# Kernel optimization log

Measured on AMD Instinct MI355X. Metric: run time of the kernel, lower is better.

## Reference

```python
import jax, jax.numpy as jnp
import numpy as np

BETA = 0.9
TH = 1.0  # snn.Leaky default threshold
SPARSITY = 0.5


@jax.custom_vjp
def spike(x):
    # Heaviside spike; surrogate (atan, alpha=2) gradient as in snntorch default
    return (x > 0).astype(x.dtype)

def _spike_fwd(x):
    return spike(x), x

def _spike_bwd(x, g):
    return (g / (1.0 + (jnp.pi * x) ** 2),)

spike.defvjp(_spike_fwd, _spike_bwd)


def setup_inputs() -> dict:
    key = jax.random.key(0)
    ks = jax.random.split(key, 6)
    T, B, NIN, NH, NOUT = 50, 512, 784, 1000, 10

    def mk_w(k, o, i):
        k1, k2 = jax.random.split(k)
        w = jax.random.normal(k1, (o, i), jnp.float32) * (1.0 / np.sqrt(i))
        mask = (jax.random.uniform(k2, (o, i)) > SPARSITY).astype(jnp.float32)
        return w * mask

    x = jax.random.normal(ks[0], (T, B, NIN), jnp.float32)
    return dict(
        x=x,
        W0=mk_w(ks[1], NH, NIN), b0=jnp.zeros((NH,), jnp.float32),
        W1=mk_w(ks[2], NH, NH), b1=jnp.zeros((NH,), jnp.float32),
        W2=mk_w(ks[3], NH, NH), b2=jnp.zeros((NH,), jnp.float32),
        W3=mk_w(ks[4], NOUT, NH), b3=jnp.zeros((NOUT,), jnp.float32),
    )


def reference(x, W0, b0, W1, b1, W2, b2, W3, b3):
    params = ((W0, b0), (W1, b1), (W2, b2), (W3, b3))
    B = x.shape[1]
    mems0 = tuple(jnp.zeros((B, W.shape[0]), x.dtype) for W, _ in params)

    def step(mems, xt):
        inp = xt
        new_mems, spks = [], []
        for (W, b), m in zip(params, mems):
            cur = inp @ W.T + b
            # snntorch Leaky (reset_mechanism='subtract'):
            # reset from previous mem (detached), then mem = beta*mem + I - reset*th
            reset = jax.lax.stop_gradient((m > TH).astype(x.dtype))
            m_new = BETA * m + cur - reset * TH
            s = spike(m_new - TH)
            new_mems.append(m_new)
            spks.append(s)
            inp = s
        return tuple(new_mems), (tuple(spks), tuple(new_mems))

    _, (spk_rec, mem_rec) = jax.lax.scan(step, mems0, x)
    # spk_rec/mem_rec: tuples of [T, B, dim] arrays per layer
    return (*spk_rec, *mem_rec)
```

## Files before the change

### kernel.cpp

```cpp
#include <hip/hip_runtime.h>


typedef int int4v  __attribute__((ext_vector_type(4)));
typedef int int16v __attribute__((ext_vector_type(16)));

#define XSCALE 68719476736.0
#define WSCALE 1099511627776.0
#define TC 10

__global__ void wsplit_i8(const float* __restrict__ W, signed char* __restrict__ out,
                          int Nreal, int Npad, int K, int Kpad)
{
    int idx = blockIdx.x * blockDim.x + threadIdx.x;
    int total = Npad * Kpad;
    if (idx >= total) return;
    int n = idx / Kpad, k = idx - n * Kpad;
    long long v = 0;
    if (n < Nreal && k < K) v = __double2ll_rn((double)W[(size_t)n * K + k] * WSCALE);
    size_t plane = (size_t)total;
#pragma unroll
    for (int p = 0; p < 4; ++p) {
        int d = (int)(v & 255); if (d > 127) d -= 256;
        out[p * plane + idx] = (signed char)d;
        v = (v - d) >> 8;
    }
    out[4 * plane + idx] = (signed char)v;
}

__global__ void xsplit_chunk(const float* __restrict__ x, signed char* __restrict__ out)
{
    int idx = blockIdx.x * blockDim.x + threadIdx.x;
    if (idx >= 5120 * 832) return;
    int row = idx / 832, k = idx - row * 832;
    long long v = 0;
    if (k < 784) v = __double2ll_rn((double)x[(size_t)row * 784 + k] * XSCALE);
    const size_t plane = (size_t)5120 * 832;
    signed char* o = out + idx;
#pragma unroll
    for (int p = 0; p < 4; ++p) {
        int d = (int)(v & 255); if (d > 127) d -= 256;
        o[p * plane] = (signed char)d;
        v = (v - d) >> 8;
    }
    o[4 * plane] = (signed char)v;
}

template<int NA, int KP, int CS>
__global__ __launch_bounds__(256)
void gemm32(const signed char* __restrict__ Ap, size_t planeA,
            const signed char* __restrict__ Wp, size_t planeW,
            double* __restrict__ curout)
{
    __shared__ __align__(16) signed char Wld[5 * 64 * 80];
    __shared__ __align__(16) signed char Ald[NA * 64 * 80];
    constexpr int NIT = KP / 64;

    const int tid = threadIdx.x;
    const int l   = tid & 63;
    const int w   = tid >> 6;
    const int wm  = (w & 1) * 32;
    const int wn  = (w >> 1) * 32;
    const int r32 = l & 31;
    const int h   = l >> 5;

    const int bm = blockIdx.y * 64;
    const int bn = blockIdx.x * 64;

    const int srow = tid >> 2;
    const int sc   = (tid & 3) * 16;

    const signed char* ag = Ap + (size_t)(bm + srow) * KP + sc;
    const signed char* wg = Wp + (size_t)(bn + srow) * KP + sc;

    int4v Ar[NA], Wr[5];
#pragma unroll
    for (int p = 0; p < 5; ++p)  Wr[p] = *(const int4v*)(wg + p * planeW);
#pragma unroll
    for (int p = 0; p < NA; ++p) Ar[p] = *(const int4v*)(ag + p * planeA);

    int16v acc[5];
#pragma unroll
    for (int s = 0; s < 5; ++s)
#pragma unroll
        for (int r = 0; r < 16; ++r) acc[s][r] = 0;

    for (int it = 0; it < NIT; ++it) {
        __syncthreads();
#pragma unroll
        for (int p = 0; p < 5; ++p)
            *(int4v*)&Wld[(p * 64 + srow) * 80 + sc] = Wr[p];
#pragma unroll
        for (int p = 0; p < NA; ++p)
            *(int4v*)&Ald[(p * 64 + srow) * 80 + sc] = Ar[p];
        __syncthreads();

        if (it + 1 < NIT) {
            int kb = (it + 1) * 64;
#pragma unroll
            for (int p = 0; p < 5; ++p)
                Wr[p] = *(const int4v*)(wg + kb + p * planeW);
#pragma unroll
            for (int p = 0; p < NA; ++p)
                Ar[p] = *(const int4v*)(ag + kb + p * planeA);
        }

#pragma unroll
        for (int k2 = 0; k2 < 2; ++k2) {
            const int off = k2 * 32 + 16 * h;
            if constexpr (NA == 5) {
                int4v af[5], bq[5];
#pragma unroll
                for (int p = 0; p < 5; ++p)
                    af[p] = *(const int4v*)&Ald[(p * 64 + wm + r32) * 80 + off];
#pragma unroll
                for (int q = 0; q < 5; ++q)
                    bq[q] = *(const int4v*)&Wld[(q * 64 + wn + r32) * 80 + off];
#pragma unroll
                for (int q = 0; q < 5; ++q)
#pragma unroll
                    for (int p = 0; p < 5; ++p)
                        if (p + q >= 4)
                            acc[p + q - 4] = __builtin_amdgcn_mfma_i32_32x32x32_i8(
                                af[p], bq[q], acc[p + q - 4], 0, 0, 0);
            } else {
                int4v a0 = *(const int4v*)&Ald[(wm + r32) * 80 + off];
#pragma unroll
                for (int q = 0; q < 5; ++q) {
                    int4v bq = *(const int4v*)&Wld[(q * 64 + wn + r32) * 80 + off];
                    acc[q] = __builtin_amdgcn_mfma_i32_32x32x32_i8(a0, bq, acc[q], 0, 0, 0);
                }
            }
        }
    }

    const int col = bn + wn + r32;
    if (col < CS) {
#pragma unroll
        for (int reg = 0; reg < 16; ++reg) {
            int row = bm + wm + (reg & 3) + 8 * (reg >> 2) + 4 * h;
            double v = (double)acc[4][reg];
            v = v * 256.0 + (double)acc[3][reg];
            v = v * 256.0 + (double)acc[2][reg];
            v = v * 256.0 + (double)acc[1][reg];
            v = v * 256.0 + (double)acc[0][reg];
            curout[(size_t)row * CS + col] = v * (NA == 5 ? 0x1p-44 : 0x1p-40);
        }
    }
}

template<int KP>
__global__ __launch_bounds__(256)
void gemm32w(const signed char* __restrict__ Asp,
             const signed char* __restrict__ Wp, size_t planeW,
             double* __restrict__ curout)
{
    __shared__ __align__(16) signed char Wld[5 * 64 * 80];
    __shared__ __align__(16) signed char Ald[128 * 80];
    constexpr int NIT = KP / 64;

    const int tid = threadIdx.x;
    const int l   = tid & 63;
    const int w   = tid >> 6;
    const int wm  = (w & 1) * 64;
    const int wn  = (w >> 1) * 32;
    const int r32 = l & 31;
    const int h   = l >> 5;

    const int bm = blockIdx.y * 128;
    const int bn = blockIdx.x * 64;

    const int srA = tid >> 1;
    const int scA = (tid & 1) * 32;
    const int srW = tid >> 2;
    const int scW = (tid & 3) * 16;

    const signed char* ag = Asp + (size_t)(bm + srA) * KP + scA;
    const signed char* wg = Wp  + (size_t)(bn + srW) * KP + scW;

    int4v Ar0 = *(const int4v*)(ag);
    int4v Ar1 = *(const int4v*)(ag + 16);
    int4v Wr[5];
#pragma unroll
    for (int p = 0; p < 5; ++p) Wr[p] = *(const int4v*)(wg + p * planeW);

    int16v acc[2][5];
#pragma unroll
    for (int mi = 0; mi < 2; ++mi)
#pragma unroll
        for (int s = 0; s < 5; ++s)
#pragma unroll
            for (int r = 0; r < 16; ++r) acc[mi][s][r] = 0;

    for (int it = 0; it < NIT; ++it) {
        __syncthreads();
#pragma unroll
        for (int p = 0; p < 5; ++p)
            *(int4v*)&Wld[(p * 64 + srW) * 80 + scW] = Wr[p];
        *(int4v*)&Ald[srA * 80 + scA]      = Ar0;
        *(int4v*)&Ald[srA * 80 + scA + 16] = Ar1;
        __syncthreads();

        if (it + 1 < NIT) {
            int kb = (it + 1) * 64;
            Ar0 = *(const int4v*)(ag + kb);
            Ar1 = *(const int4v*)(ag + kb + 16);
#pragma unroll
            for (int p = 0; p < 5; ++p)
                Wr[p] = *(const int4v*)(wg + kb + p * planeW);
        }

#pragma unroll
        for (int k2 = 0; k2 < 2; ++k2) {
            const int off = k2 * 32 + 16 * h;
            int4v bq[5];
#pragma unroll
            for (int q = 0; q < 5; ++q)
                bq[q] = *(const int4v*)&Wld[(q * 64 + wn + r32) * 80 + off];
#pragma unroll
            for (int mi = 0; mi < 2; ++mi) {
                int4v a0 = *(const int4v*)&Ald[(wm + mi * 32 + r32) * 80 + off];
#pragma unroll
                for (int q = 0; q < 5; ++q)
                    acc[mi][q] = __builtin_amdgcn_mfma_i32_32x32x32_i8(
                        a0, bq[q], acc[mi][q], 0, 0, 0);
            }
        }
    }

    const int col = bn + wn + r32;
#pragma unroll
    for (int mi = 0; mi < 2; ++mi)
#pragma unroll
        for (int reg = 0; reg < 16; ++reg) {
            int row = bm + wm + mi * 32 + (reg & 3) + 8 * (reg >> 2) + 4 * h;
            double v = (double)acc[mi][4][reg];
            v = v * 256.0 + (double)acc[mi][3][reg];
            v = v * 256.0 + (double)acc[mi][2][reg];
            v = v * 256.0 + (double)acc[mi][1][reg];
            v = v * 256.0 + (double)acc[mi][0][reg];
            curout[(size_t)row * 1024 + col] = v * 0x1p-40;
        }
}

__global__ __launch_bounds__(256)
void if_update(const double* __restrict__ cur, const float* __restrict__ bias,
               double* __restrict__ mw, float* __restrict__ spk,
               float* __restrict__ mem, signed char* __restrict__ spk_i8,
               int first)
{
    int idx = blockIdx.x * blockDim.x + threadIdx.x;
    if (idx >= 512 * 500) return;
    int row = idx / 500, col = (idx - row * 500) * 2;
    double2 mp = first ? make_double2(0.0, 0.0)
                       : *(const double2*)&mw[(size_t)row * 1000 + col];
    double bs0 = (double)bias[col], bs1 = (double)bias[col + 1];
#pragma unroll 2
    for (int t = 0; t < TC; ++t) {
        double2 c = *(const double2*)&cur[((size_t)t * 512 + row) * 1024 + col];
        double rst0 = (mp.x > 1.0) ? 1.0 : 0.0;
        double rst1 = (mp.y > 1.0) ? 1.0 : 0.0;
        double mn0 = 0.9 * mp.x + (c.x + bs0) - rst0;
        double mn1 = 0.9 * mp.y + (c.y + bs1) - rst1;
        int s0 = (mn0 > 1.0) ? 1 : 0;
        int s1 = (mn1 > 1.0) ? 1 : 0;
        size_t o = ((size_t)t * 512 + row) * 1000 + col;
        *(float2*)&spk[o] = make_float2((float)s0, (float)s1);
        *(float2*)&mem[o] = make_float2((float)mn0, (float)mn1);
        *(short*)&spk_i8[((size_t)t * 512 + row) * 1024 + col] =
            (short)(s0 | (s1 << 8));
        mp.x = mn0; mp.y = mn1;
    }
    *(double2*)&mw[(size_t)row * 1000 + col] = mp;
}

__global__ __launch_bounds__(256)
void if3_kernel(const double* __restrict__ cur3, const float* __restrict__ bias,
                float* __restrict__ spk3, float* __restrict__ mem3)
{
    int idx = blockIdx.x * blockDim.x + threadIdx.x;
    if (idx >= 5120) return;
    int brow = idx / 10, col = idx - brow * 10;
    double bs = (double)bias[col];
    double mp = 0.0;
    for (int t = 0; t < 50; ++t) {
        double c   = cur3[((size_t)t * 512 + brow) * 16 + col] + bs;
        double rst = (mp > 1.0) ? 1.0 : 0.0;
        double mn  = 0.9 * mp + c - rst;
        size_t o   = (size_t)t * 5120 + (size_t)brow * 10 + col;
        spk3[o] = (mn > 1.0) ? 1.0f : 0.0f;
        mem3[o] = (float)mn;
        mp = mn;
    }
}

extern "C" void kernel_launch(void* const* d_in, const int* in_sizes, int n_in,
                              void* d_out, int out_size, void* d_ws, size_t ws_size,
                              hipStream_t stream)
{
    const float* x  = (const float*)d_in[0];
    const float* W0 = (const float*)d_in[1];
    const float* b0 = (const float*)d_in[2];
    const float* W1 = (const float*)d_in[3];
    const float* b1 = (const float*)d_in[4];
    const float* W2 = (const float*)d_in[5];
    const float* b2 = (const float*)d_in[6];
    const float* W3 = (const float*)d_in[7];
    const float* b3 = (const float*)d_in[8];
    float* out = (float*)d_out;

    const int T = 50;
    const size_t LNH = (size_t)512 * 1000;
    const size_t LNO = (size_t)512 * 10;

    float* spk0 = out;
    float* spk1 = spk0 + (size_t)T * LNH;
    float* spk2 = spk1 + (size_t)T * LNH;
    float* spk3 = spk2 + (size_t)T * LNH;
    float* mem0 = spk3 + (size_t)T * LNO;
    float* mem1 = mem0 + (size_t)T * LNH;
    float* mem2 = mem1 + (size_t)T * LNH;
    float* mem3 = mem2 + (size_t)T * LNH;

    double* cur = (double*)d_ws;
    double* mw0 = cur + (size_t)5120 * 1024;
    double* mw1 = mw0 + LNH;
    double* mw2 = mw1 + LNH;
    signed char* W0d = (signed char*)(mw2 + LNH);
    signed char* W1d = W0d + (size_t)5 * 1024 * 832;
    signed char* W2d = W1d + (size_t)5 * 1024 * 1024;
    signed char* W3d = W2d + (size_t)5 * 1024 * 1024;
    signed char* xsb = W3d + (size_t)5 * 64 * 1024;
    signed char* sp0 = xsb + (size_t)5 * 5120 * 832;
    signed char* sp1 = sp0 + (size_t)5120 * 1024;
    signed char* sp2 = sp1 + (size_t)5120 * 1024;

    hipMemsetAsync(sp0, 0, (size_t)2 * 5120 * 1024 + (size_t)25600 * 1024, stream);

    wsplit_i8<<<(1024 * 832  + 255) / 256, 256, 0, stream>>>(W0, W0d, 1000, 1024, 784,  832);
    wsplit_i8<<<(1024 * 1024 + 255) / 256, 256, 0, stream>>>(W1, W1d, 1000, 1024, 1000, 1024);
    wsplit_i8<<<(1024 * 1024 + 255) / 256, 256, 0, stream>>>(W2, W2d, 1000, 1024, 1000, 1024);
    wsplit_i8<<<(64 * 1024   + 255) / 256, 256, 0, stream>>>(W3, W3d, 10,   64,   1000, 1024);

    const size_t plA0 = (size_t)5120 * 832;
    const size_t plW0 = (size_t)1024 * 832;
    const size_t plWH = (size_t)1024 * 1024;
    const size_t plW3 = (size_t)64 * 1024;

    dim3 blk(256);
    dim3 g0(16, 80);
    dim3 gW(16, 40);
    dim3 g3(1, 400);

    for (int c = 0; c < T / TC; ++c) {
        const int t0 = c * TC;
        const int first = (c == 0);

        xsplit_chunk<<<(5120 * 832 + 255) / 256, 256, 0, stream>>>(
            x + (size_t)t0 * 512 * 784, xsb);

        gemm32<5, 832, 1024><<<g0, blk, 0, stream>>>(xsb, plA0, W0d, plW0, cur);
        if_update<<<1000, 256, 0, stream>>>(cur, b0, mw0,
            spk0 + (size_t)t0 * LNH, mem0 + (size_t)t0 * LNH, sp0, first);

        gemm32w<1024><<<gW, blk, 0, stream>>>(sp0, W1d, plWH, cur);
        if_update<<<1000, 256, 0, stream>>>(cur, b1, mw1,
            spk1 + (size_t)t0 * LNH, mem1 + (size_t)t0 * LNH, sp1, first);

        gemm32w<1024><<<gW, blk, 0, stream>>>(sp1, W2d, plWH, cur);
        if_update<<<1000, 256, 0, stream>>>(cur, b2, mw2,
            spk2 + (size_t)t0 * LNH, mem2 + (size_t)t0 * LNH,
            sp2 + (size_t)t0 * 512 * 1024, first);
    }

    gemm32<1, 1024, 16><<<g3, blk, 0, stream>>>(sp2, 0, W3d, plW3, cur);
    if3_kernel<<<20, 256, 0, stream>>>(cur, b3, spk3, mem3);
}
```

Measured before the change: 1.102 ms.

## Process all timesteps per layer in one pass instead of time chunks

Removes the 10-timestep chunk loop and runs each layer's GEMM over all 25600 rows at once, followed by a single membrane update kernel that scans all 50 timesteps. This cuts kernel launches and the saved-membrane round trips, and gives each GEMM a much larger grid for better occupancy. The cost is a much larger workspace for the fp64 current buffer and the split input, which adds memory traffic and footprint. The update kernel now runs a 50-step serial loop per thread with no unrolling.

New measurement: 1.060 ms. 3.8% less time.

```diff
diff --git a/kernel.cpp b/kernel.cpp
--- a/kernel.cpp
+++ b/kernel.cpp
@@ -6,7 +6,7 @@
 
 #define XSCALE 68719476736.0
 #define WSCALE 1099511627776.0
-#define TC 10
+#define MT 25600
 
 __global__ void wsplit_i8(const float* __restrict__ W, signed char* __restrict__ out,
                           int Nreal, int Npad, int K, int Kpad)
@@ -27,14 +27,14 @@
     out[4 * plane + idx] = (signed char)v;
 }
 
-__global__ void xsplit_chunk(const float* __restrict__ x, signed char* __restrict__ out)
+__global__ void xsplit_all(const float* __restrict__ x, signed char* __restrict__ out)
 {
     int idx = blockIdx.x * blockDim.x + threadIdx.x;
-    if (idx >= 5120 * 832) return;
+    if (idx >= MT * 832) return;
     int row = idx / 832, k = idx - row * 832;
     long long v = 0;
     if (k < 784) v = __double2ll_rn((double)x[(size_t)row * 784 + k] * XSCALE);
-    const size_t plane = (size_t)5120 * 832;
+    const size_t plane = (size_t)MT * 832;
     signed char* o = out + idx;
 #pragma unroll
     for (int p = 0; p < 4; ++p) {
@@ -244,23 +244,20 @@
 
 __global__ __launch_bounds__(256)
 void if_update(const double* __restrict__ cur, const float* __restrict__ bias,
-               double* __restrict__ mw, float* __restrict__ spk,
-               float* __restrict__ mem, signed char* __restrict__ spk_i8,
-               int first)
+               float* __restrict__ spk, float* __restrict__ mem,
+               signed char* __restrict__ spk_i8)
 {
     int idx = blockIdx.x * blockDim.x + threadIdx.x;
     if (idx >= 512 * 500) return;
     int row = idx / 500, col = (idx - row * 500) * 2;
-    double2 mp = first ? make_double2(0.0, 0.0)
-                       : *(const double2*)&mw[(size_t)row * 1000 + col];
+    double mp0 = 0.0, mp1 = 0.0;
     double bs0 = (double)bias[col], bs1 = (double)bias[col + 1];
-#pragma unroll 2
-    for (int t = 0; t < TC; ++t) {
+    for (int t = 0; t < 50; ++t) {
         double2 c = *(const double2*)&cur[((size_t)t * 512 + row) * 1024 + col];
-        double rst0 = (mp.x > 1.0) ? 1.0 : 0.0;
-        double rst1 = (mp.y > 1.0) ? 1.0 : 0.0;
-        double mn0 = 0.9 * mp.x + (c.x + bs0) - rst0;
-        double mn1 = 0.9 * mp.y + (c.y + bs1) - rst1;
+        double rst0 = (mp0 > 1.0) ? 1.0 : 0.0;
+        double rst1 = (mp1 > 1.0) ? 1.0 : 0.0;
+        double mn0 = 0.9 * mp0 + (c.x + bs0) - rst0;
+        double mn1 = 0.9 * mp1 + (c.y + bs1) - rst1;
         int s0 = (mn0 > 1.0) ? 1 : 0;
         int s1 = (mn1 > 1.0) ? 1 : 0;
         size_t o = ((size_t)t * 512 + row) * 1000 + col;
@@ -268,9 +265,8 @@
         *(float2*)&mem[o] = make_float2((float)mn0, (float)mn1);
         *(short*)&spk_i8[((size_t)t * 512 + row) * 1024 + col] =
             (short)(s0 | (s1 << 8));
-        mp.x = mn0; mp.y = mn1;
-    }
-    *(double2*)&mw[(size_t)row * 1000 + col] = mp;
+        mp0 = mn0; mp1 = mn1;
+    }
 }
 
 __global__ __launch_bounds__(256)
@@ -322,56 +318,40 @@
     float* mem3 = mem2 + (size_t)T * LNH;
 
     double* cur = (double*)d_ws;
-    double* mw0 = cur + (size_t)5120 * 1024;
-    double* mw1 = mw0 + LNH;
-    double* mw2 = mw1 + LNH;
-    signed char* W0d = (signed char*)(mw2 + LNH);
+    signed char* W0d = (signed char*)(cur + (size_t)MT * 1024);
     signed char* W1d = W0d + (size_t)5 * 1024 * 832;
     signed char* W2d = W1d + (size_t)5 * 1024 * 1024;
     signed char* W3d = W2d + (size_t)5 * 1024 * 1024;
     signed char* xsb = W3d + (size_t)5 * 64 * 1024;
-    signed char* sp0 = xsb + (size_t)5 * 5120 * 832;
-    signed char* sp1 = sp0 + (size_t)5120 * 1024;
-    signed char* sp2 = sp1 + (size_t)5120 * 1024;
-
-    hipMemsetAsync(sp0, 0, (size_t)2 * 5120 * 1024 + (size_t)25600 * 1024, stream);
+    signed char* sp0 = xsb + (size_t)5 * MT * 832;
+    signed char* sp1 = sp0 + (size_t)MT * 1024;
+    signed char* sp2 = sp1 + (size_t)MT * 1024;
+
+    hipMemsetAsync(sp0, 0, (size_t)3 * MT * 1024, stream);
 
     wsplit_i8<<<(1024 * 832  + 255) / 256, 256, 0, stream>>>(W0, W0d, 1000, 1024, 784,  832);
     wsplit_i8<<<(1024 * 1024 + 255) / 256, 256, 0, stream>>>(W1, W1d, 1000, 1024, 1000, 1024);
     wsplit_i8<<<(1024 * 1024 + 255) / 256, 256, 0, stream>>>(W2, W2d, 1000, 1024, 1000, 1024);
     wsplit_i8<<<(64 * 1024   + 255) / 256, 256, 0, stream>>>(W3, W3d, 10,   64,   1000, 1024);
 
-    const size_t plA0 = (size_t)5120 * 832;
+    xsplit_all<<<(MT * 832 + 255) / 256, 256, 0, stream>>>(x, xsb);
+
+    const size_t plA0 = (size_t)MT * 832;
     const size_t plW0 = (size_t)1024 * 832;
     const size_t plWH = (size_t)1024 * 1024;
     const size_t plW3 = (size_t)64 * 1024;
 
     dim3 blk(256);
-    dim3 g0(16, 80);
-    dim3 gW(16, 40);
-    dim3 g3(1, 400);
-
-    for (int c = 0; c < T / TC; ++c) {
-        const int t0 = c * TC;
-        const int first = (c == 0);
-
-        xsplit_chunk<<<(5120 * 832 + 255) / 256, 256, 0, stream>>>(
-            x + (size_t)t0 * 512 * 784, xsb);
-
-        gemm32<5, 832, 1024><<<g0, blk, 0, stream>>>(xsb, plA0, W0d, plW0, cur);
-        if_update<<<1000, 256, 0, stream>>>(cur, b0, mw0,
-            spk0 + (size_t)t0 * LNH, mem0 + (size_t)t0 * LNH, sp0, first);
-
-        gemm32w<1024><<<gW, blk, 0, stream>>>(sp0, W1d, plWH, cur);
-        if_update<<<1000, 256, 0, stream>>>(cur, b1, mw1,
-            spk1 + (size_t)t0 * LNH, mem1 + (size_t)t0 * LNH, sp1, first);
-
-        gemm32w<1024><<<gW, blk, 0, stream>>>(sp1, W2d, plWH, cur);
-        if_update<<<1000, 256, 0, stream>>>(cur, b2, mw2,
-            spk2 + (size_t)t0 * LNH, mem2 + (size_t)t0 * LNH,
-            sp2 + (size_t)t0 * 512 * 1024, first);
-    }
-
+    dim3 g0(16, MT / 64);
+    dim3 gW(16, MT / 128);
+    dim3 g3(1, MT / 64);
+
+    gemm32<5, 832, 1024><<<g0, blk, 0, stream>>>(xsb, plA0, W0d, plW0, cur);
+    if_update<<<1000, 256, 0, stream>>>(cur, b0, spk0, mem0, sp0);
+    gemm32w<1024><<<gW, blk, 0, stream>>>(sp0, W1d, plWH, cur);
+    if_update<<<1000, 256, 0, stream>>>(cur, b1, spk1, mem1, sp1);
+    gemm32w<1024><<<gW, blk, 0, stream>>>(sp1, W2d, plWH, cur);
+    if_update<<<1000, 256, 0, stream>>>(cur, b2, spk2, mem2, sp2);
     gemm32<1, 1024, 16><<<g3, blk, 0, stream>>>(sp2, 0, W3d, plW3, cur);
     if3_kernel<<<20, 256, 0, stream>>>(cur, b3, spk3, mem3);
 }
```
